# Performance work log

Hardware: AMD Instinct MI355X
Metric: run time of the kernel (lower is better)

The kernel has to match this reference:

```python
import jax, jax.numpy as jnp
import numpy as np

B, D, R, E, L = 8192, 2048, 64, 4, 3


def setup_inputs() -> dict:
    key = jax.random.key(0)
    ks = jax.random.split(key, 6)
    inputs = jax.random.normal(ks[0], (B, D), dtype=jnp.float32)
    # xavier-normal-ish init for low-rank factors
    U = jax.random.normal(ks[1], (L, E, D, R), dtype=jnp.float32) * (2.0 / (D + R)) ** 0.5
    V = jax.random.normal(ks[2], (L, E, D, R), dtype=jnp.float32) * (2.0 / (D + R)) ** 0.5
    C = jax.random.normal(ks[3], (L, E, R, R), dtype=jnp.float32) * (1.0 / R) ** 0.5
    gate_w = jax.random.normal(ks[4], (E, D), dtype=jnp.float32) * (1.0 / D) ** 0.5
    bias = jnp.zeros((L, D), dtype=jnp.float32)
    return {"inputs": inputs, "U": U, "V": V, "C": C, "gate_w": gate_w, "bias": bias}


def reference(inputs, U, V, C, gate_w, bias):
    x0 = inputs                      # (B, D)
    x_l = inputs
    for i in range(L):
        # gating scores per expert, softmax over experts
        gs = jax.nn.softmax(x_l @ gate_w.T, axis=-1)            # (B, E)
        # low-rank cross: tanh(V^T x) -> tanh(C .) -> U .
        vx = jnp.tanh(jnp.einsum('edr,bd->ber', V[i], x_l))     # (B, E, R)
        cx = jnp.tanh(jnp.einsum('esr,ber->bes', C[i], vx))     # (B, E, R)
        uv = jnp.einsum('eds,bes->bed', U[i], cx)               # (B, E, D)
        dot = (uv + bias[i][None, None, :]) * x0[:, None, :]    # (B, E, D)
        x_l = jnp.einsum('bed,be->bd', dot, gs) + x_l           # MoE combine + residual
    return x_l
```

## Files before the change

kernel.cpp:

```cpp
#include <hip/hip_runtime.h>
#include <cmath>

#define Bb 8192
#define Dd 2048
#define Rr 64
#define Ee 4
#define Ll 3

typedef __bf16 bf16x8 __attribute__((ext_vector_type(8)));
typedef float f32x4 __attribute__((ext_vector_type(4)));
typedef unsigned short u16x8 __attribute__((ext_vector_type(8)));
typedef unsigned short u16x4 __attribute__((ext_vector_type(4)));

__device__ __forceinline__ unsigned short f2bf(float f){
  unsigned u = __builtin_bit_cast(unsigned, f);
  u += 0x7fffu + ((u >> 16) & 1u);
  return (unsigned short)(u >> 16);
}
__device__ __forceinline__ float bf2f(unsigned short h){
  return __builtin_bit_cast(float, ((unsigned)h) << 16);
}

__global__ __launch_bounds__(256) void prep_w_k(const float* __restrict__ U,
                                                const float* __restrict__ V,
                                                const float* __restrict__ C,
                                                const float* __restrict__ gw,
                                                unsigned short* __restrict__ VfT,
                                                unsigned short* __restrict__ UfT,
                                                unsigned short* __restrict__ cb16,
                                                unsigned short* __restrict__ gw16){
  const int NV = Ll * 256 * Dd;
  const int NU = Ll * Dd * 256;
  const int NC = Ll * Ee * Rr * Rr;
  const int NG = Ee * Dd;
  const int total = NV + NU + NC + NG;
  for (int idx = blockIdx.x * blockDim.x + threadIdx.x; idx < total; idx += gridDim.x * blockDim.x){
    if (idx < NV){
      int l = idx / (256 * Dd); int rem = idx - l * 256 * Dd;
      int n = rem / Dd, d = rem - n * Dd;
      int e = n >> 6, r = n & 63;
      VfT[idx] = f2bf(V[(((size_t)l * Ee + e) * Dd + d) * Rr + r]);
    } else if (idx < NV + NU){
      int j = idx - NV;
      int l = j / (Dd * 256); int rem = j - l * Dd * 256;
      int d = rem / 256, k = rem - d * 256;
      int e = k >> 6, s = k & 63;
      UfT[j] = f2bf(U[(((size_t)l * Ee + e) * Dd + d) * Rr + s]);
    } else if (idx < NV + NU + NC){
      int j = idx - NV - NU;
      cb16[j] = f2bf(C[j]);
    } else {
      int j = idx - NV - NU - NC;
      gw16[j] = f2bf(gw[j]);
    }
  }
}

__global__ __launch_bounds__(256) void cast_gate_k(const float* __restrict__ x,
                                                   unsigned short* __restrict__ xb0,
                                                   const unsigned short* __restrict__ gw16,
                                                   float* __restrict__ gs){
  const int lane = threadIdx.x & 63;
  const int w = threadIdx.x >> 6;
  const int row = blockIdx.x * 4 + w;
  float s0 = 0.f, s1 = 0.f, s2 = 0.f, s3 = 0.f;
  #pragma unroll
  for (int c = 0; c < 4; c++){
    const int k = c * 512 + lane * 8;
    const float* xr = x + (size_t)row * Dd + k;
    f32x4 v0 = *(const f32x4*)xr;
    f32x4 v1 = *(const f32x4*)(xr + 4);
    float xf[8];
    u16x8 ob;
    #pragma unroll
    for (int u = 0; u < 4; u++){
      xf[u] = v0[u]; xf[4 + u] = v1[u];
      ob[u] = f2bf(v0[u]); ob[4 + u] = f2bf(v1[u]);
    }
    *(u16x8*)(xb0 + (size_t)row * Dd + k) = ob;
    u16x8 g0v = *(const u16x8*)(gw16 + 0 * Dd + k);
    u16x8 g1v = *(const u16x8*)(gw16 + 1 * Dd + k);
    u16x8 g2v = *(const u16x8*)(gw16 + 2 * Dd + k);
    u16x8 g3v = *(const u16x8*)(gw16 + 3 * Dd + k);
    #pragma unroll
    for (int u = 0; u < 8; u++){
      s0 += xf[u] * bf2f(g0v[u]);
      s1 += xf[u] * bf2f(g1v[u]);
      s2 += xf[u] * bf2f(g2v[u]);
      s3 += xf[u] * bf2f(g3v[u]);
    }
  }
  #pragma unroll
  for (int m = 1; m < 64; m <<= 1){
    s0 += __shfl_xor(s0, m, 64);
    s1 += __shfl_xor(s1, m, 64);
    s2 += __shfl_xor(s2, m, 64);
    s3 += __shfl_xor(s3, m, 64);
  }
  if (lane == 0){
    float mx = fmaxf(fmaxf(s0, s1), fmaxf(s2, s3));
    float e0 = __expf(s0 - mx), e1 = __expf(s1 - mx), e2 = __expf(s2 - mx), e3 = __expf(s3 - mx);
    float inv = 1.f / (e0 + e1 + e2 + e3);
    f32x4 g; g[0] = e0 * inv; g[1] = e1 * inv; g[2] = e2 * inv; g[3] = e3 * inv;
    *(f32x4*)(gs + (size_t)row * 4) = g;
  }
}

__global__ __launch_bounds__(256) void gate_k(const float* __restrict__ xv,
                                              const unsigned short* __restrict__ gw16,
                                              float* __restrict__ gs){
  const int lane = threadIdx.x & 63;
  const int w = threadIdx.x >> 6;
  const int row = blockIdx.x * 4 + w;
  float s0 = 0.f, s1 = 0.f, s2 = 0.f, s3 = 0.f;
  #pragma unroll
  for (int c = 0; c < 4; c++){
    const int k = c * 512 + lane * 8;
    const float* xr = xv + (size_t)row * Dd + k;
    f32x4 v0 = *(const f32x4*)xr;
    f32x4 v1 = *(const f32x4*)(xr + 4);
    float xf[8];
    #pragma unroll
    for (int u = 0; u < 4; u++){ xf[u] = v0[u]; xf[4 + u] = v1[u]; }
    u16x8 g0v = *(const u16x8*)(gw16 + 0 * Dd + k);
    u16x8 g1v = *(const u16x8*)(gw16 + 1 * Dd + k);
    u16x8 g2v = *(const u16x8*)(gw16 + 2 * Dd + k);
    u16x8 g3v = *(const u16x8*)(gw16 + 3 * Dd + k);
    #pragma unroll
    for (int u = 0; u < 8; u++){
      s0 += xf[u] * bf2f(g0v[u]);
      s1 += xf[u] * bf2f(g1v[u]);
      s2 += xf[u] * bf2f(g2v[u]);
      s3 += xf[u] * bf2f(g3v[u]);
    }
  }
  #pragma unroll
  for (int m = 1; m < 64; m <<= 1){
    s0 += __shfl_xor(s0, m, 64);
    s1 += __shfl_xor(s1, m, 64);
    s2 += __shfl_xor(s2, m, 64);
    s3 += __shfl_xor(s3, m, 64);
  }
  if (lane == 0){
    float mx = fmaxf(fmaxf(s0, s1), fmaxf(s2, s3));
    float e0 = __expf(s0 - mx), e1 = __expf(s1 - mx), e2 = __expf(s2 - mx), e3 = __expf(s3 - mx);
    float inv = 1.f / (e0 + e1 + e2 + e3);
    f32x4 g; g[0] = e0 * inv; g[1] = e1 * inv; g[2] = e2 * inv; g[3] = e3 * inv;
    *(f32x4*)(gs + (size_t)row * 4) = g;
  }
}

template<bool AF32>
__global__ __launch_bounds__(256) void gemm1_k(const void* __restrict__ Av,
                                               const unsigned short* __restrict__ BT,
                                               unsigned short* __restrict__ vxp){
  const int bm0 = blockIdx.x * 64;
  const int bn0 = blockIdx.y * 128;
  const int z   = blockIdx.z;
  const int kc0 = z * 512;
  const int tid = threadIdx.x;
  const int lane = tid & 63;
  const int wv = tid >> 6;
  const int wm = wv >> 1, wn = wv & 1;

  __shared__ __align__(16) char smraw[27648];
  unsigned short (*As)[72] = (unsigned short (*)[72])smraw;
  unsigned short (*Bs)[72] = (unsigned short (*)[72])(smraw + 9216);
  float (*epi)[132] = (float (*)[132])smraw;

  f32x4 acc[2][4] = {};
  const int arow = tid >> 2;
  const int aseg = tid & 3;

  const float* Af = (const float*)Av;
  const unsigned short* Ab = (const unsigned short*)Av;

  f32x4 a4[4]; u16x8 ar[2]; u16x8 br[4];
  if constexpr (AF32){
    #pragma unroll
    for (int j = 0; j < 4; j++)
      a4[j] = *(const f32x4*)(Af + (size_t)(bm0 + arow) * Dd + kc0 + aseg * 16 + j * 4);
  } else {
    ar[0] = *(const u16x8*)(Ab + (size_t)(bm0 + arow) * Dd + kc0 + aseg * 16);
    ar[1] = *(const u16x8*)(Ab + (size_t)(bm0 + arow) * Dd + kc0 + aseg * 16 + 8);
  }
  br[0] = *(const u16x8*)(BT + (size_t)(bn0 + arow) * Dd + kc0 + aseg * 16);
  br[1] = *(const u16x8*)(BT + (size_t)(bn0 + arow) * Dd + kc0 + aseg * 16 + 8);
  br[2] = *(const u16x8*)(BT + (size_t)(bn0 + arow + 64) * Dd + kc0 + aseg * 16);
  br[3] = *(const u16x8*)(BT + (size_t)(bn0 + arow + 64) * Dd + kc0 + aseg * 16 + 8);

  for (int k0 = kc0; k0 < kc0 + 512; k0 += 64){
    __syncthreads();
    if constexpr (AF32){
      u16x8 av0, av1;
      #pragma unroll
      for (int j = 0; j < 4; j++){
        av0[j] = f2bf(a4[0][j]); av0[4 + j] = f2bf(a4[1][j]);
        av1[j] = f2bf(a4[2][j]); av1[4 + j] = f2bf(a4[3][j]);
      }
      *(u16x8*)(&As[arow][aseg * 16])     = av0;
      *(u16x8*)(&As[arow][aseg * 16 + 8]) = av1;
    } else {
      *(u16x8*)(&As[arow][aseg * 16])     = ar[0];
      *(u16x8*)(&As[arow][aseg * 16 + 8]) = ar[1];
    }
    *(u16x8*)(&Bs[arow][aseg * 16])          = br[0];
    *(u16x8*)(&Bs[arow][aseg * 16 + 8])      = br[1];
    *(u16x8*)(&Bs[arow + 64][aseg * 16])     = br[2];
    *(u16x8*)(&Bs[arow + 64][aseg * 16 + 8]) = br[3];
    __syncthreads();

    int kn = k0 + 64;
    if (kn < kc0 + 512){
      if constexpr (AF32){
        #pragma unroll
        for (int j = 0; j < 4; j++)
          a4[j] = *(const f32x4*)(Af + (size_t)(bm0 + arow) * Dd + kn + aseg * 16 + j * 4);
      } else {
        ar[0] = *(const u16x8*)(Ab + (size_t)(bm0 + arow) * Dd + kn + aseg * 16);
        ar[1] = *(const u16x8*)(Ab + (size_t)(bm0 + arow) * Dd + kn + aseg * 16 + 8);
      }
      br[0] = *(const u16x8*)(BT + (size_t)(bn0 + arow) * Dd + kn + aseg * 16);
      br[1] = *(const u16x8*)(BT + (size_t)(bn0 + arow) * Dd + kn + aseg * 16 + 8);
      br[2] = *(const u16x8*)(BT + (size_t)(bn0 + arow + 64) * Dd + kn + aseg * 16);
      br[3] = *(const u16x8*)(BT + (size_t)(bn0 + arow + 64) * Dd + kn + aseg * 16 + 8);
    }

    #pragma unroll
    for (int ks = 0; ks < 2; ks++){
      bf16x8 af[2];
      #pragma unroll
      for (int mi = 0; mi < 2; mi++)
        af[mi] = *reinterpret_cast<const bf16x8*>(&As[wm * 32 + mi * 16 + (lane & 15)][ks * 32 + (lane >> 4) * 8]);
      #pragma unroll
      for (int nj = 0; nj < 4; nj++){
        bf16x8 bfr = *reinterpret_cast<const bf16x8*>(&Bs[wn * 64 + nj * 16 + (lane & 15)][ks * 32 + (lane >> 4) * 8]);
        #pragma unroll
        for (int mi = 0; mi < 2; mi++)
          acc[mi][nj] = __builtin_amdgcn_mfma_f32_16x16x32_bf16(af[mi], bfr, acc[mi][nj], 0, 0, 0);
      }
    }
  }

  unsigned short* outz = vxp + (size_t)z * Bb * 256;
  #pragma unroll
  for (int h = 0; h < 2; h++){
    __syncthreads();
    if (wm == h){
      #pragma unroll
      for (int mi = 0; mi < 2; mi++)
        #pragma unroll
        for (int nj = 0; nj < 4; nj++)
          #pragma unroll
          for (int q = 0; q < 4; q++)
            epi[mi * 16 + (lane >> 4) * 4 + q][wn * 64 + nj * 16 + (lane & 15)] = acc[mi][nj][q];
    }
    __syncthreads();
    #pragma unroll
    for (int c = 0; c < 4; c++){
      int idx = c * 256 + tid;
      int r = idx >> 5;
      int col = (idx & 31) * 4;
      f32x4 v = *(const f32x4*)&epi[r][col];
      u16x4 ov;
      #pragma unroll
      for (int j = 0; j < 4; j++) ov[j] = f2bf(v[j]);
      *(u16x4*)(outz + (size_t)(bm0 + h * 32 + r) * 256 + bn0 + col) = ov;
    }
  }
}

template<bool FROMPLOG>
__global__ __launch_bounds__(256) void gemm2_k(const unsigned short* __restrict__ vxp,
                                               const unsigned short* __restrict__ cb,
                                               const float* __restrict__ gsb,
                                               const float* __restrict__ plog,
                                               unsigned short* __restrict__ wb){
  const int bm0 = blockIdx.x * 64;
  const int e   = blockIdx.y;
  const int tid = threadIdx.x;
  const int lane = tid & 63;
  const int wv = tid >> 6;
  const int wm = wv >> 1, wn = wv & 1;

  __shared__ __align__(16) char smraw[19456];
  unsigned short (*As)[72] = (unsigned short (*)[72])smraw;
  unsigned short (*Bs)[72] = (unsigned short (*)[72])(smraw + 9216);
  float (*gs_l)[4] = (float (*)[4])(smraw + 18432);
  unsigned short (*epi)[72] = (unsigned short (*)[72])smraw;

  if constexpr (FROMPLOG){
    int r = tid >> 2, q = tid & 3;
    f32x4 s = {0.f, 0.f, 0.f, 0.f};
    #pragma unroll
    for (int ci = 0; ci < 4; ci++)
      s += *(const f32x4*)(plog + ((size_t)(q * 4 + ci) * Bb + bm0 + r) * 4);
    #pragma unroll
    for (int j = 0; j < 4; j++){
      s[j] += __shfl_xor(s[j], 1, 64);
      s[j] += __shfl_xor(s[j], 2, 64);
    }
    if (q == 0){
      float mx = fmaxf(fmaxf(s[0], s[1]), fmaxf(s[2], s[3]));
      float e0 = __expf(s[0] - mx), e1 = __expf(s[1] - mx), e2 = __expf(s[2] - mx), e3 = __expf(s[3] - mx);
      float inv = 1.f / (e0 + e1 + e2 + e3);
      f32x4 g; g[0] = e0 * inv; g[1] = e1 * inv; g[2] = e2 * inv; g[3] = e3 * inv;
      *(f32x4*)&gs_l[r][0] = g;
    }
  } else {
    if (tid < 64) *(f32x4*)&gs_l[tid][0] = *(const f32x4*)(gsb + (size_t)(bm0 + tid) * 4);
  }

  const int arow = tid >> 2;
  const int aseg = tid & 3;

  float tv[16];
  #pragma unroll
  for (int j = 0; j < 16; j++) tv[j] = 0.f;
  #pragma unroll
  for (int z = 0; z < 4; z++){
    const unsigned short* vz = vxp + ((size_t)z * Bb + bm0 + arow) * 256 + e * 64 + aseg * 16;
    u16x8 p0 = *(const u16x8*)vz;
    u16x8 p1 = *(const u16x8*)(vz + 8);
    #pragma unroll
    for (int j = 0; j < 8; j++){ tv[j] += bf2f(p0[j]); tv[8 + j] += bf2f(p1[j]); }
  }
  u16x8 av0, av1;
  #pragma unroll
  for (int j = 0; j < 4; j++){
    av0[j] = f2bf(tanhf(tv[j]));     av0[4 + j] = f2bf(tanhf(tv[4 + j]));
    av1[j] = f2bf(tanhf(tv[8 + j])); av1[4 + j] = f2bf(tanhf(tv[12 + j]));
  }
  *(u16x8*)(&As[arow][aseg * 16]) = av0;
  *(u16x8*)(&As[arow][aseg * 16 + 8]) = av1;
  *(u16x8*)(&Bs[arow][aseg * 16])     = *(const u16x8*)(cb + e * 4096 + arow * 64 + aseg * 16);
  *(u16x8*)(&Bs[arow][aseg * 16 + 8]) = *(const u16x8*)(cb + e * 4096 + arow * 64 + aseg * 16 + 8);
  __syncthreads();

  f32x4 acc[2][2] = {};
  #pragma unroll
  for (int kk = 0; kk < 2; kk++){
    bf16x8 af[2];
    #pragma unroll
    for (int mi = 0; mi < 2; mi++)
      af[mi] = *reinterpret_cast<const bf16x8*>(&As[wm * 32 + mi * 16 + (lane & 15)][kk * 32 + (lane >> 4) * 8]);
    #pragma unroll
    for (int nj = 0; nj < 2; nj++){
      bf16x8 bfr = *reinterpret_cast<const bf16x8*>(&Bs[wn * 32 + nj * 16 + (lane & 15)][kk * 32 + (lane >> 4) * 8]);
      #pragma unroll
      for (int mi = 0; mi < 2; mi++)
        acc[mi][nj] = __builtin_amdgcn_mfma_f32_16x16x32_bf16(af[mi], bfr, acc[mi][nj], 0, 0, 0);
    }
  }

  __syncthreads();
  #pragma unroll
  for (int mi = 0; mi < 2; mi++)
    #pragma unroll
    for (int nj = 0; nj < 2; nj++)
      #pragma unroll
      for (int q = 0; q < 4; q++){
        int row = wm * 32 + mi * 16 + (lane >> 4) * 4 + q;
        int col = wn * 32 + nj * 16 + (lane & 15);
        float g = gs_l[row][e];
        epi[row][col] = f2bf(g * tanhf(acc[mi][nj][q]));
      }
  __syncthreads();
  #pragma unroll
  for (int c = 0; c < 2; c++){
    int idx = c * 256 + tid;
    int row = idx >> 3;
    int col = (idx & 7) * 8;
    *(u16x8*)(wb + (size_t)(bm0 + row) * 256 + e * 64 + col) = *(const u16x8*)(&epi[row][col]);
  }
}

template<int MODE, bool X0BF>
__global__ __launch_bounds__(256, 3) void gemm3_k(const unsigned short* __restrict__ A,
                                                  const unsigned short* __restrict__ BT,
                                                  const float* __restrict__ x0f,
                                                  const unsigned short* __restrict__ x0b,
                                                  unsigned short* __restrict__ xst,
                                                  const float* __restrict__ biasrow,
                                                  float* __restrict__ out,
                                                  const unsigned short* __restrict__ gw16,
                                                  float* __restrict__ plog){
  const int bm0 = blockIdx.x * 128;
  const int bn0 = blockIdx.y * 128;
  const int tid = threadIdx.x;
  const int lane = tid & 63;
  const int wv = tid >> 6;
  const int wm = wv >> 1, wn = wv & 1;

  __shared__ __align__(16) char smraw[20480];
  unsigned short (*As)[40] = (unsigned short (*)[40])smraw;
  unsigned short (*Bs)[40] = (unsigned short (*)[40])(smraw + 10240);
  float (*epi)[132] = (float (*)[132])smraw;

  f32x4 acc[4][4] = {};
  const int arow = tid >> 2;
  const int aseg = tid & 3;

  u16x8 ar0 = *(const u16x8*)(A + (size_t)(bm0 + arow) * 256 + aseg * 8);
  u16x8 ar1 = *(const u16x8*)(A + (size_t)(bm0 + arow + 64) * 256 + aseg * 8);
  u16x8 br0 = *(const u16x8*)(BT + (size_t)(bn0 + arow) * 256 + aseg * 8);
  u16x8 br1 = *(const u16x8*)(BT + (size_t)(bn0 + arow + 64) * 256 + aseg * 8);

  for (int k0 = 0; k0 < 256; k0 += 32){
    __syncthreads();
    *(u16x8*)(&As[arow][aseg * 8])      = ar0;
    *(u16x8*)(&As[arow + 64][aseg * 8]) = ar1;
    *(u16x8*)(&Bs[arow][aseg * 8])      = br0;
    *(u16x8*)(&Bs[arow + 64][aseg * 8]) = br1;
    __syncthreads();
    if (k0 + 32 < 256){
      ar0 = *(const u16x8*)(A + (size_t)(bm0 + arow) * 256 + k0 + 32 + aseg * 8);
      ar1 = *(const u16x8*)(A + (size_t)(bm0 + arow + 64) * 256 + k0 + 32 + aseg * 8);
      br0 = *(const u16x8*)(BT + (size_t)(bn0 + arow) * 256 + k0 + 32 + aseg * 8);
      br1 = *(const u16x8*)(BT + (size_t)(bn0 + arow + 64) * 256 + k0 + 32 + aseg * 8);
    }
    bf16x8 af[4];
    #pragma unroll
    for (int mi = 0; mi < 4; mi++)
      af[mi] = *reinterpret_cast<const bf16x8*>(&As[wm * 64 + mi * 16 + (lane & 15)][(lane >> 4) * 8]);
    #pragma unroll
    for (int nj = 0; nj < 4; nj++){
      bf16x8 bfr = *reinterpret_cast<const bf16x8*>(&Bs[wn * 64 + nj * 16 + (lane & 15)][(lane >> 4) * 8]);
      #pragma unroll
      for (int mi = 0; mi < 4; mi++)
        acc[mi][nj] = __builtin_amdgcn_mfma_f32_16x16x32_bf16(af[mi], bfr, acc[mi][nj], 0, 0, 0);
    }
  }

  u16x4 x0p[2][4]; u16x4 xsp[2][4]; f32x4 x0q[2][4];
  (void)x0p; (void)xsp; (void)x0q;

#define PRE_LOADS(H, S)                                                        \
  {                                                                            \
    _Pragma("unroll")                                                          \
    for (int c = 0; c < 4; c++){                                               \
      int idx = c * 256 + tid;                                                 \
      int r = idx >> 5, col = (idx & 31) * 4;                                  \
      size_t o = (size_t)(bm0 + (H) * 32 + r) * Dd + bn0 + col;                \
      if constexpr (X0BF) x0p[S][c] = *(const u16x4*)(x0b + o);                \
      else                x0q[S][c] = *(const f32x4*)(x0f + o);                \
      if constexpr (MODE != 0) xsp[S][c] = *(const u16x4*)(xst + o);           \
    }                                                                          \
  }

  PRE_LOADS(0, 0)

  #pragma unroll
  for (int h = 0; h < 4; h++){
    __syncthreads();
    if (wm == (h >> 1)){
      const int mib = (h & 1) * 2;
      #pragma unroll
      for (int m2 = 0; m2 < 2; m2++)
        #pragma unroll
        for (int nj = 0; nj < 4; nj++)
          #pragma unroll
          for (int q = 0; q < 4; q++)
            epi[m2 * 16 + (lane >> 4) * 4 + q][wn * 64 + nj * 16 + (lane & 15)] = acc[mib + m2][nj][q];
    }
    if (h == 0) PRE_LOADS(1, 1)
    else if (h == 1) PRE_LOADS(2, 0)
    else if (h == 2) PRE_LOADS(3, 1)
    __syncthreads();
    const int hb = h & 1;
    #pragma unroll
    for (int c = 0; c < 4; c++){
      int idx = c * 256 + tid;
      int r = idx >> 5;
      int col = (idx & 31) * 4;
      int row = bm0 + h * 32 + r;
      size_t o = (size_t)row * Dd + bn0 + col;
      f32x4 y = *(const f32x4*)&epi[r][col];
      f32x4 bv = *(const f32x4*)(biasrow + bn0 + col);
      f32x4 x0v;
      if constexpr (X0BF){
        u16x4 xv = x0p[hb][c];
        #pragma unroll
        for (int j = 0; j < 4; j++) x0v[j] = bf2f(xv[j]);
      } else {
        x0v = x0q[hb][c];
      }
      f32x4 xo;
      if constexpr (MODE == 0){
        xo = x0v;
      } else {
        u16x4 xv = xsp[hb][c];
        #pragma unroll
        for (int j = 0; j < 4; j++) xo[j] = bf2f(xv[j]);
      }
      f32x4 xn;
      #pragma unroll
      for (int j = 0; j < 4; j++) xn[j] = xo[j] + x0v[j] * (bv[j] + y[j]);
      if constexpr (MODE == 2){
        *(f32x4*)(out + o) = xn;
      } else {
        u16x4 xnb;
        #pragma unroll
        for (int j = 0; j < 4; j++) xnb[j] = f2bf(xn[j]);
        *(u16x4*)(xst + o) = xnb;
      }
      if constexpr (MODE != 2){
        float s[4];
        #pragma unroll
        for (int e = 0; e < 4; e++){
          u16x4 gv = *(const u16x4*)(gw16 + (size_t)e * Dd + bn0 + col);
          s[e] = xn[0] * bf2f(gv[0]) + xn[1] * bf2f(gv[1])
               + xn[2] * bf2f(gv[2]) + xn[3] * bf2f(gv[3]);
        }
        #pragma unroll
        for (int m = 1; m < 32; m <<= 1)
          #pragma unroll
          for (int e = 0; e < 4; e++) s[e] += __shfl_xor(s[e], m, 64);
        if ((tid & 31) == 0){
          f32x4 pv; pv[0] = s[0]; pv[1] = s[1]; pv[2] = s[2]; pv[3] = s[3];
          *(f32x4*)(plog + ((size_t)blockIdx.y * Bb + row) * 4) = pv;
        }
      }
    }
  }
#undef PRE_LOADS
}

extern "C" void kernel_launch(void* const* d_in, const int* in_sizes, int n_in,
                              void* d_out, int out_size, void* d_ws, size_t ws_size,
                              hipStream_t stream){
  (void)in_sizes; (void)n_in; (void)out_size;
  const float* inp  = (const float*)d_in[0];
  const float* U    = (const float*)d_in[1];
  const float* V    = (const float*)d_in[2];
  const float* C    = (const float*)d_in[3];
  const float* gw   = (const float*)d_in[4];
  const float* bias = (const float*)d_in[5];
  float* out = (float*)d_out;

  char* ws = (char*)d_ws;
  size_t o = 0;
  unsigned short* xb  = (unsigned short*)(ws + o); o += (size_t)Bb * Dd * 2;
  unsigned short* vxp = (unsigned short*)(ws + o); o += (size_t)4 * Bb * 256 * 2;
  unsigned short* wb  = (unsigned short*)(ws + o); o += (size_t)Bb * 256 * 2;
  float*          gsb = (float*)(ws + o);          o += (size_t)Bb * 4 * 4;
  float*          plog= (float*)(ws + o);          o += (size_t)16 * Bb * 4 * 4;
  unsigned short* vft = (unsigned short*)(ws + o); o += (size_t)Ll * 256 * Dd * 2;
  unsigned short* uft = (unsigned short*)(ws + o); o += (size_t)Ll * Dd * 256 * 2;
  unsigned short* cb16= (unsigned short*)(ws + o); o += (size_t)Ll * Ee * Rr * Rr * 2;
  unsigned short* g16 = (unsigned short*)(ws + o); o += (size_t)Ee * Dd * 2;
  if (ws_size < o) return;
  unsigned short* x0b = nullptr;
  if (ws_size >= o + (size_t)Bb * Dd * 2){
    x0b = (unsigned short*)(ws + o); o += (size_t)Bb * Dd * 2;
  }
  const bool hx = (x0b != nullptr);

  prep_w_k<<<1024, 256, 0, stream>>>(U, V, C, gw, vft, uft, cb16, g16);
  if (hx) cast_gate_k<<<Bb / 4, 256, 0, stream>>>(inp, x0b, g16, gsb);

  for (int l = 0; l < Ll; l++){
    const unsigned short* vftl = vft + (size_t)l * 256 * Dd;
    const unsigned short* uftl = uft + (size_t)l * Dd * 256;
    const unsigned short* cbl  = cb16 + (size_t)l * Ee * Rr * Rr;
    const float* biasl = bias + (size_t)l * Dd;

    if (l == 0){
      if (hx){
        gemm1_k<false><<<dim3(Bb / 64, 2, 4), 256, 0, stream>>>(x0b, vftl, vxp);
      } else {
        gate_k<<<Bb / 4, 256, 0, stream>>>(inp, g16, gsb);
        gemm1_k<true><<<dim3(Bb / 64, 2, 4), 256, 0, stream>>>(inp, vftl, vxp);
      }
      gemm2_k<false><<<dim3(Bb / 64, Ee), 256, 0, stream>>>(vxp, cbl, gsb, plog, wb);
    } else {
      gemm1_k<false><<<dim3(Bb / 64, 2, 4), 256, 0, stream>>>(xb, vftl, vxp);
      gemm2_k<true><<<dim3(Bb / 64, Ee), 256, 0, stream>>>(vxp, cbl, gsb, plog, wb);
    }

    dim3 g3(Bb / 128, Dd / 128);
    if (l == 0){
      if (hx) gemm3_k<0, true ><<<g3, 256, 0, stream>>>(wb, uftl, inp, x0b, xb, biasl, out, g16, plog);
      else    gemm3_k<0, false><<<g3, 256, 0, stream>>>(wb, uftl, inp, x0b, xb, biasl, out, g16, plog);
    } else if (l == 1){
      if (hx) gemm3_k<1, true ><<<g3, 256, 0, stream>>>(wb, uftl, inp, x0b, xb, biasl, out, g16, plog);
      else    gemm3_k<1, false><<<g3, 256, 0, stream>>>(wb, uftl, inp, x0b, xb, biasl, out, g16, plog);
    } else {
      if (hx) gemm3_k<2, true ><<<g3, 256, 0, stream>>>(wb, uftl, inp, x0b, xb, biasl, out, g16, plog);
      else    gemm3_k<2, false><<<g3, 256, 0, stream>>>(wb, uftl, inp, x0b, xb, biasl, out, g16, plog);
    }
  }
}
```

Before: 215.2 us.

## Split GEMM3 epilogue into separate bf16 Y GEMM and row-wise combine kernel

```diff
diff --git a/kernel.cpp b/kernel.cpp
--- a/kernel.cpp
+++ b/kernel.cpp
@@ -270,11 +270,9 @@
   }
 }
 
-template<bool FROMPLOG>
 __global__ __launch_bounds__(256) void gemm2_k(const unsigned short* __restrict__ vxp,
                                                const unsigned short* __restrict__ cb,
                                                const float* __restrict__ gsb,
-                                               const float* __restrict__ plog,
                                                unsigned short* __restrict__ wb){
   const int bm0 = blockIdx.x * 64;
   const int e   = blockIdx.y;
@@ -289,27 +287,7 @@
   float (*gs_l)[4] = (float (*)[4])(smraw + 18432);
   unsigned short (*epi)[72] = (unsigned short (*)[72])smraw;
 
-  if constexpr (FROMPLOG){
-    int r = tid >> 2, q = tid & 3;
-    f32x4 s = {0.f, 0.f, 0.f, 0.f};
-    #pragma unroll
-    for (int ci = 0; ci < 4; ci++)
-      s += *(const f32x4*)(plog + ((size_t)(q * 4 + ci) * Bb + bm0 + r) * 4);
-    #pragma unroll
-    for (int j = 0; j < 4; j++){
-      s[j] += __shfl_xor(s[j], 1, 64);
-      s[j] += __shfl_xor(s[j], 2, 64);
-    }
-    if (q == 0){
-      float mx = fmaxf(fmaxf(s[0], s[1]), fmaxf(s[2], s[3]));
-      float e0 = __expf(s[0] - mx), e1 = __expf(s[1] - mx), e2 = __expf(s[2] - mx), e3 = __expf(s[3] - mx);
-      float inv = 1.f / (e0 + e1 + e2 + e3);
-      f32x4 g; g[0] = e0 * inv; g[1] = e1 * inv; g[2] = e2 * inv; g[3] = e3 * inv;
-      *(f32x4*)&gs_l[r][0] = g;
-    }
-  } else {
-    if (tid < 64) *(f32x4*)&gs_l[tid][0] = *(const f32x4*)(gsb + (size_t)(bm0 + tid) * 4);
-  }
+  if (tid < 64) *(f32x4*)&gs_l[tid][0] = *(const f32x4*)(gsb + (size_t)(bm0 + tid) * 4);
 
   const int arow = tid >> 2;
   const int aseg = tid & 3;
@@ -375,16 +353,9 @@
   }
 }
 
-template<int MODE, bool X0BF>
-__global__ __launch_bounds__(256, 3) void gemm3_k(const unsigned short* __restrict__ A,
-                                                  const unsigned short* __restrict__ BT,
-                                                  const float* __restrict__ x0f,
-                                                  const unsigned short* __restrict__ x0b,
-                                                  unsigned short* __restrict__ xst,
-                                                  const float* __restrict__ biasrow,
-                                                  float* __restrict__ out,
-                                                  const unsigned short* __restrict__ gw16,
-                                                  float* __restrict__ plog){
+__global__ __launch_bounds__(256, 4) void gemm_y_k(const unsigned short* __restrict__ A,
+                                                   const unsigned short* __restrict__ BT,
+                                                   unsigned short* __restrict__ ybf){
   const int bm0 = blockIdx.x * 128;
   const int bn0 = blockIdx.y * 128;
   const int tid = threadIdx.x;
@@ -432,24 +403,6 @@
     }
   }
 
-  u16x4 x0p[2][4]; u16x4 xsp[2][4]; f32x4 x0q[2][4];
-  (void)x0p; (void)xsp; (void)x0q;
-
-#define PRE_LOADS(H, S)                                                        \
-  {                                                                            \
-    _Pragma("unroll")                                                          \
-    for (int c = 0; c < 4; c++){                                               \
-      int idx = c * 256 + tid;                                                 \
-      int r = idx >> 5, col = (idx & 31) * 4;                                  \
-      size_t o = (size_t)(bm0 + (H) * 32 + r) * Dd + bn0 + col;                \
-      if constexpr (X0BF) x0p[S][c] = *(const u16x4*)(x0b + o);                \
-      else                x0q[S][c] = *(const f32x4*)(x0f + o);                \
-      if constexpr (MODE != 0) xsp[S][c] = *(const u16x4*)(xst + o);           \
-    }                                                                          \
-  }
-
-  PRE_LOADS(0, 0)
-
   #pragma unroll
   for (int h = 0; h < 4; h++){
     __syncthreads();
@@ -463,67 +416,108 @@
           for (int q = 0; q < 4; q++)
             epi[m2 * 16 + (lane >> 4) * 4 + q][wn * 64 + nj * 16 + (lane & 15)] = acc[mib + m2][nj][q];
     }
-    if (h == 0) PRE_LOADS(1, 1)
-    else if (h == 1) PRE_LOADS(2, 0)
-    else if (h == 2) PRE_LOADS(3, 1)
-    __syncthreads();
-    const int hb = h & 1;
-    #pragma unroll
-    for (int c = 0; c < 4; c++){
+    __syncthreads();
+    #pragma unroll
+    for (int c = 0; c < 2; c++){
       int idx = c * 256 + tid;
-      int r = idx >> 5;
-      int col = (idx & 31) * 4;
-      int row = bm0 + h * 32 + r;
-      size_t o = (size_t)row * Dd + bn0 + col;
-      f32x4 y = *(const f32x4*)&epi[r][col];
-      f32x4 bv = *(const f32x4*)(biasrow + bn0 + col);
-      f32x4 x0v;
-      if constexpr (X0BF){
-        u16x4 xv = x0p[hb][c];
-        #pragma unroll
-        for (int j = 0; j < 4; j++) x0v[j] = bf2f(xv[j]);
-      } else {
-        x0v = x0q[hb][c];
+      int r = idx >> 4;
+      int col = (idx & 15) * 8;
+      f32x4 v0 = *(const f32x4*)&epi[r][col];
+      f32x4 v1 = *(const f32x4*)&epi[r][col + 4];
+      u16x8 ov;
+      #pragma unroll
+      for (int j = 0; j < 4; j++){ ov[j] = f2bf(v0[j]); ov[4 + j] = f2bf(v1[j]); }
+      *(u16x8*)(ybf + (size_t)(bm0 + h * 32 + r) * Dd + bn0 + col) = ov;
+    }
+  }
+}
+
+template<int MODE, bool X0BF>
+__global__ __launch_bounds__(256) void combine_k(const unsigned short* __restrict__ ybf,
+                                                 const float* __restrict__ x0f,
+                                                 const unsigned short* __restrict__ x0b,
+                                                 unsigned short* __restrict__ xst,
+                                                 const float* __restrict__ biasrow,
+                                                 float* __restrict__ out,
+                                                 const unsigned short* __restrict__ gw16,
+                                                 float* __restrict__ gs){
+  const int lane = threadIdx.x & 63;
+  const int w = threadIdx.x >> 6;
+  const int row = blockIdx.x * 4 + w;
+  float s0 = 0.f, s1 = 0.f, s2 = 0.f, s3 = 0.f;
+  #pragma unroll
+  for (int c = 0; c < 4; c++){
+    const int k = c * 512 + lane * 8;
+    size_t o = (size_t)row * Dd + k;
+    u16x8 yv = *(const u16x8*)(ybf + o);
+    f32x4 b0 = *(const f32x4*)(biasrow + k);
+    f32x4 b1 = *(const f32x4*)(biasrow + k + 4);
+    float x0v[8];
+    if constexpr (X0BF){
+      u16x8 xv = *(const u16x8*)(x0b + o);
+      #pragma unroll
+      for (int j = 0; j < 8; j++) x0v[j] = bf2f(xv[j]);
+    } else {
+      f32x4 v0 = *(const f32x4*)(x0f + o);
+      f32x4 v1 = *(const f32x4*)(x0f + o + 4);
+      #pragma unroll
+      for (int j = 0; j < 4; j++){ x0v[j] = v0[j]; x0v[4 + j] = v1[j]; }
+    }
+    float xo[8];
+    if constexpr (MODE == 0){
+      #pragma unroll
+      for (int j = 0; j < 8; j++) xo[j] = x0v[j];
+    } else {
+      u16x8 sv = *(const u16x8*)(xst + o);
+      #pragma unroll
+      for (int j = 0; j < 8; j++) xo[j] = bf2f(sv[j]);
+    }
+    float xn[8];
+    #pragma unroll
+    for (int j = 0; j < 4; j++){
+      xn[j]     = xo[j]     + x0v[j]     * (b0[j] + bf2f(yv[j]));
+      xn[4 + j] = xo[4 + j] + x0v[4 + j] * (b1[j] + bf2f(yv[4 + j]));
+    }
+    if constexpr (MODE == 2){
+      f32x4 o0, o1;
+      #pragma unroll
+      for (int j = 0; j < 4; j++){ o0[j] = xn[j]; o1[j] = xn[4 + j]; }
+      *(f32x4*)(out + o) = o0;
+      *(f32x4*)(out + o + 4) = o1;
+    } else {
+      u16x8 nv;
+      #pragma unroll
+      for (int j = 0; j < 8; j++) nv[j] = f2bf(xn[j]);
+      *(u16x8*)(xst + o) = nv;
+      u16x8 g0v = *(const u16x8*)(gw16 + 0 * Dd + k);
+      u16x8 g1v = *(const u16x8*)(gw16 + 1 * Dd + k);
+      u16x8 g2v = *(const u16x8*)(gw16 + 2 * Dd + k);
+      u16x8 g3v = *(const u16x8*)(gw16 + 3 * Dd + k);
+      #pragma unroll
+      for (int j = 0; j < 8; j++){
+        s0 += xn[j] * bf2f(g0v[j]);
+        s1 += xn[j] * bf2f(g1v[j]);
+        s2 += xn[j] * bf2f(g2v[j]);
+        s3 += xn[j] * bf2f(g3v[j]);
       }
-      f32x4 xo;
-      if constexpr (MODE == 0){
-        xo = x0v;
-      } else {
-        u16x4 xv = xsp[hb][c];
-        #pragma unroll
-        for (int j = 0; j < 4; j++) xo[j] = bf2f(xv[j]);
-      }
-      f32x4 xn;
-      #pragma unroll
-      for (int j = 0; j < 4; j++) xn[j] = xo[j] + x0v[j] * (bv[j] + y[j]);
-      if constexpr (MODE == 2){
-        *(f32x4*)(out + o) = xn;
-      } else {
-        u16x4 xnb;
-        #pragma unroll
-        for (int j = 0; j < 4; j++) xnb[j] = f2bf(xn[j]);
-        *(u16x4*)(xst + o) = xnb;
-      }
-      if constexpr (MODE != 2){
-        float s[4];
-        #pragma unroll
-        for (int e = 0; e < 4; e++){
-          u16x4 gv = *(const u16x4*)(gw16 + (size_t)e * Dd + bn0 + col);
-          s[e] = xn[0] * bf2f(gv[0]) + xn[1] * bf2f(gv[1])
-               + xn[2] * bf2f(gv[2]) + xn[3] * bf2f(gv[3]);
-        }
-        #pragma unroll
-        for (int m = 1; m < 32; m <<= 1)
-          #pragma unroll
-          for (int e = 0; e < 4; e++) s[e] += __shfl_xor(s[e], m, 64);
-        if ((tid & 31) == 0){
-          f32x4 pv; pv[0] = s[0]; pv[1] = s[1]; pv[2] = s[2]; pv[3] = s[3];
-          *(f32x4*)(plog + ((size_t)blockIdx.y * Bb + row) * 4) = pv;
-        }
-      }
-    }
-  }
-#undef PRE_LOADS
+    }
+  }
+  if constexpr (MODE != 2){
+    #pragma unroll
+    for (int m = 1; m < 64; m <<= 1){
+      s0 += __shfl_xor(s0, m, 64);
+      s1 += __shfl_xor(s1, m, 64);
+      s2 += __shfl_xor(s2, m, 64);
+      s3 += __shfl_xor(s3, m, 64);
+    }
+    if (lane == 0){
+      float mx = fmaxf(fmaxf(s0, s1), fmaxf(s2, s3));
+      float e0 = __expf(s0 - mx), e1 = __expf(s1 - mx), e2 = __expf(s2 - mx), e3 = __expf(s3 - mx);
+      float inv = 1.f / (e0 + e1 + e2 + e3);
+      f32x4 g; g[0] = e0 * inv; g[1] = e1 * inv; g[2] = e2 * inv; g[3] = e3 * inv;
+      *(f32x4*)(gs + (size_t)row * 4) = g;
+    }
+  }
 }
 
 extern "C" void kernel_launch(void* const* d_in, const int* in_sizes, int n_in,
@@ -543,8 +537,8 @@
   unsigned short* xb  = (unsigned short*)(ws + o); o += (size_t)Bb * Dd * 2;
   unsigned short* vxp = (unsigned short*)(ws + o); o += (size_t)4 * Bb * 256 * 2;
   unsigned short* wb  = (unsigned short*)(ws + o); o += (size_t)Bb * 256 * 2;
+  unsigned short* ybf = (unsigned short*)(ws + o); o += (size_t)Bb * Dd * 2;
   float*          gsb = (float*)(ws + o);          o += (size_t)Bb * 4 * 4;
-  float*          plog= (float*)(ws + o);          o += (size_t)16 * Bb * 4 * 4;
   unsigned short* vft = (unsigned short*)(ws + o); o += (size_t)Ll * 256 * Dd * 2;
   unsigned short* uft = (unsigned short*)(ws + o); o += (size_t)Ll * Dd * 256 * 2;
   unsigned short* cb16= (unsigned short*)(ws + o); o += (size_t)Ll * Ee * Rr * Rr * 2;
@@ -558,6 +552,7 @@
 
   prep_w_k<<<1024, 256, 0, stream>>>(U, V, C, gw, vft, uft, cb16, g16);
   if (hx) cast_gate_k<<<Bb / 4, 256, 0, stream>>>(inp, x0b, g16, gsb);
+  else    gate_k<<<Bb / 4, 256, 0, stream>>>(inp, g16, gsb);
 
   for (int l = 0; l < Ll; l++){
     const unsigned short* vftl = vft + (size_t)l * 256 * Dd;
@@ -566,28 +561,24 @@
     const float* biasl = bias + (size_t)l * Dd;
 
     if (l == 0){
-      if (hx){
-        gemm1_k<false><<<dim3(Bb / 64, 2, 4), 256, 0, stream>>>(x0b, vftl, vxp);
-      } else {
-        gate_k<<<Bb / 4, 256, 0, stream>>>(inp, g16, gsb);
-        gemm1_k<true><<<dim3(Bb / 64, 2, 4), 256, 0, stream>>>(inp, vftl, vxp);
-      }
-      gemm2_k<false><<<dim3(Bb / 64, Ee), 256, 0, stream>>>(vxp, cbl, gsb, plog, wb);
+      if (hx) gemm1_k<false><<<dim3(Bb / 64, 2, 4), 256, 0, stream>>>(x0b, vftl, vxp);
+      else    gemm1_k<true ><<<dim3(Bb / 64, 2, 4), 256, 0, stream>>>(inp, vftl, vxp);
     } else {
       gemm1_k<false><<<dim3(Bb / 64, 2, 4), 256, 0, stream>>>(xb, vftl, vxp);
-      gemm2_k<true><<<dim3(Bb / 64, Ee), 256, 0, stream>>>(vxp, cbl, gsb, plog, wb);
-    }
-
-    dim3 g3(Bb / 128, Dd / 128);
+    }
+    gemm2_k<<<dim3(Bb / 64, Ee), 256, 0, stream>>>(vxp, cbl, gsb, wb);
+    gemm_y_k<<<dim3(Bb / 128, Dd / 128), 256, 0, stream>>>(wb, uftl, ybf);
+
+    dim3 gc(Bb / 4);
     if (l == 0){
-      if (hx) gemm3_k<0, true ><<<g3, 256, 0, stream>>>(wb, uftl, inp, x0b, xb, biasl, out, g16, plog);
-      else    gemm3_k<0, false><<<g3, 256, 0, stream>>>(wb, uftl, inp, x0b, xb, biasl, out, g16, plog);
+      if (hx) combine_k<0, true ><<<gc, 256, 0, stream>>>(ybf, inp, x0b, xb, biasl, out, g16, gsb);
+      else    combine_k<0, false><<<gc, 256, 0, stream>>>(ybf, inp, x0b, xb, biasl, out, g16, gsb);
     } else if (l == 1){
-      if (hx) gemm3_k<1, true ><<<g3, 256, 0, stream>>>(wb, uftl, inp, x0b, xb, biasl, out, g16, plog);
-      else    gemm3_k<1, false><<<g3, 256, 0, stream>>>(wb, uftl, inp, x0b, xb, biasl, out, g16, plog);
-    } else {
-      if (hx) gemm3_k<2, true ><<<g3, 256, 0, stream>>>(wb, uftl, inp, x0b, xb, biasl, out, g16, plog);
-      else    gemm3_k<2, false><<<g3, 256, 0, stream>>>(wb, uftl, inp, x0b, xb, biasl, out, g16, plog);
-    }
-  }
-}
+      if (hx) combine_k<1, true ><<<gc, 256, 0, stream>>>(ybf, inp, x0b, xb, biasl, out, g16, gsb);
+      else    combine_k<1, false><<<gc, 256, 0, stream>>>(ybf, inp, x0b, xb, biasl, out, g16, gsb);
+    } else {
+      if (hx) combine_k<2, true ><<<gc, 256, 0, stream>>>(ybf, inp, x0b, xb, biasl, out, g16, gsb);
+      else    combine_k<2, false><<<gc, 256, 0, stream>>>(ybf, inp, x0b, xb, biasl, out, g16, gsb);
+    }
+  }
+}
```

New measurement: 228.1 us. +6.0%, slower.
